# Kernel tuning notes

Hardware: AMD Instinct MI355X
Metric: run time of the kernel (lower is better)

The kernel has to match this reference:

```python
import jax, jax.numpy as jnp
import numpy as np

NG, NL, NCAM, NP, ED = 8, 4, 6, 7, 256  # groups, levels, cams, key points, embed dims
GD = ED // NG
FIX_SCALE = jnp.array([[0.0, 0.0, 0.0], [0.45, 0.0, 0.0], [-0.45, 0.0, 0.0],
                       [0.0, 0.45, 0.0], [0.0, -0.45, 0.0], [0.0, 0.0, 0.45],
                       [0.0, 0.0, -0.45]], dtype=jnp.float32)


def grid_sample_bilinear(feat, grid):
    """feat [N,C,H,W], grid [N,A,P,2] in [-1,1]; bilinear, zeros padding, align_corners=False."""
    N, C, H, W = feat.shape
    A, P = grid.shape[1], grid.shape[2]
    gx = (grid[..., 0] + 1.0) * (W * 0.5) - 0.5
    gy = (grid[..., 1] + 1.0) * (H * 0.5) - 0.5
    x0 = jnp.floor(gx)
    y0 = jnp.floor(gy)
    wx1 = gx - x0
    wy1 = gy - y0
    feat_flat = feat.reshape(N, C, H * W)

    def gather(xi, yi, w):
        valid = (xi >= 0) & (xi <= W - 1) & (yi >= 0) & (yi <= H - 1)
        xc = jnp.clip(xi, 0, W - 1).astype(jnp.int32)
        yc = jnp.clip(yi, 0, H - 1).astype(jnp.int32)
        idx = (yc * W + xc).reshape(N, 1, A * P)
        vals = jnp.take_along_axis(feat_flat, idx, axis=2)  # [N,C,A*P]
        return vals * (w * valid).reshape(N, 1, A * P)

    out = (gather(x0, y0, (1.0 - wx1) * (1.0 - wy1))
           + gather(x0 + 1.0, y0, wx1 * (1.0 - wy1))
           + gather(x0, y0 + 1.0, (1.0 - wx1) * wy1)
           + gather(x0 + 1.0, y0 + 1.0, wx1 * wy1))
    return out.reshape(N, C, A, P)


def _forward(instance_feature, anchor, anchor_embed, feat0, feat1, feat2, feat3,
             projection_mat, image_wh, w_fc, b_fc, w_out, b_out):
    B, A = anchor.shape[:2]
    # --- key point generation (box_code_size=8: size + yaw rotation + translation) ---
    size = jnp.exp(anchor[..., 3:6])[:, :, None, :]           # [B,A,1,3]
    kp = FIX_SCALE * size                                      # [B,A,7,3]
    sin, cos = anchor[..., 6], anchor[..., 7]
    z = jnp.zeros_like(cos)
    o = jnp.ones_like(cos)
    rot = jnp.stack([jnp.stack([cos, -sin, z], -1),
                     jnp.stack([sin, cos, z], -1),
                     jnp.stack([z, z, o], -1)], -2)            # [B,A,3,3]
    kp = jnp.einsum('baij,bapj->bapi', rot, kp) + anchor[..., None, 0:3]

    # --- attention weights: softmax over cams*levels*pts per group ---
    feature = instance_feature + anchor_embed
    w = feature @ w_fc.T + b_fc                                # [B,A,NG*NCAM*NL*NP]
    w = jax.nn.softmax(w.reshape(B, A, NCAM * NL * NP, NG), axis=2)
    w = w.reshape(B, A, NCAM, NL, NP, NG)

    # --- project key points to normalized image coords ---
    pts = jnp.concatenate([kp, jnp.ones_like(kp[..., :1])], -1)  # [B,A,7,4]
    p2d = jnp.einsum('bcij,bapj->bcapi', projection_mat, pts)[..., :3]
    xy = p2d[..., :2] / jnp.maximum(p2d[..., 2:3], 1e-5)
    xy = xy / jnp.maximum(image_wh[:, :, None, None], 1e-5)
    grid = (xy * 2.0 - 1.0).reshape(B * NCAM, A, NP, 2)

    # --- multilevel bilinear sampling ---
    levels = [feat0, feat1, feat2, feat3]
    sampled = jnp.stack([grid_sample_bilinear(f.reshape((B * NCAM,) + f.shape[2:]), grid)
                         for f in levels], axis=1)             # [B*Ncam,NL,C,A,P]
    feats = sampled.reshape(B, NCAM, NL, ED, A, NP).transpose(0, 4, 1, 2, 5, 3)  # [B,A,Ncam,NL,P,C]
    feats = feats.reshape(B, A, NCAM, NL, NP, NG, GD)

    # --- weighted fusion over cams, levels, then sum over key points ---
    fused = jnp.einsum('bacnpgd,bacnpg->bagd', feats, w).reshape(B, A, ED)
    return fused @ w_out.T + b_out


def setup_inputs() -> dict:
    ks = jax.random.split(jax.random.key(0), 13)
    B, A = 2, 900
    return {
        'instance_feature': jax.random.normal(ks[0], (B, A, ED), jnp.float32),
        'anchor': jax.random.normal(ks[1], (B, A, 8), jnp.float32),
        'anchor_embed': jax.random.normal(ks[2], (B, A, ED), jnp.float32),
        'feat0': jax.random.normal(ks[3], (B, NCAM, ED, 64, 176), jnp.float32),
        'feat1': jax.random.normal(ks[4], (B, NCAM, ED, 32, 88), jnp.float32),
        'feat2': jax.random.normal(ks[5], (B, NCAM, ED, 16, 44), jnp.float32),
        'feat3': jax.random.normal(ks[6], (B, NCAM, ED, 8, 22), jnp.float32),
        'projection_mat': jax.random.normal(ks[7], (B, NCAM, 4, 4), jnp.float32),
        'image_wh': jnp.ones((B, NCAM, 2), jnp.float32),
        'w_fc': jax.random.normal(ks[8], (NG * NCAM * NL * NP, ED), jnp.float32) * 0.02,
        'b_fc': jax.random.normal(ks[9], (NG * NCAM * NL * NP,), jnp.float32) * 0.02,
        'w_out': jax.random.normal(ks[10], (ED, ED), jnp.float32) * 0.02,
        'b_out': jax.random.normal(ks[11], (ED,), jnp.float32) * 0.02,
    }


def reference(instance_feature, anchor, anchor_embed, feat0, feat1, feat2, feat3,
              projection_mat, image_wh, w_fc, b_fc, w_out, b_out):
    return _forward(instance_feature, anchor, anchor_embed, feat0, feat1, feat2, feat3,
                    projection_mat, image_wh, w_fc, b_fc, w_out, b_out)
```

## Files before the change

### kernel.cpp

```cpp
#include <hip/hip_runtime.h>
#include <math.h>

constexpr int B = 2, A = 900, ED = 256, NG = 8, NCAM = 6, NL = 4, NP = 7;
constexpr int NJ = NG * NCAM * NL * NP;
constexpr int NBA = B * A;
constexpr int NE = NCAM * NL * NP;
constexpr int SPLIT = 2;
constexpr int EHALF = NE / SPLIT;

constexpr int NFCB = 225 * 7;
constexpr int TPB  = 935;
constexpr int NTRB = TPB * B * NCAM;

typedef float nfloat4 __attribute__((ext_vector_type(4)));

__constant__ float FIXS[NP][3] = {
  {0.f,0.f,0.f},{0.45f,0.f,0.f},{-0.45f,0.f,0.f},
  {0.f,0.45f,0.f},{0.f,-0.45f,0.f},{0.f,0.f,0.45f},{0.f,0.f,-0.45f}};

__constant__ int cH[NL]  = {64,32,16,8};
__constant__ int cW[NL]  = {176,88,44,22};
__constant__ int cHW[NL] = {11264,2816,704,176};
__constant__ long long cLOFF[NL] = {0LL, 34603008LL, 43253760LL, 45416448LL};

__global__ __launch_bounds__(256) void k_prep(
    const float* __restrict__ f0, const float* __restrict__ f1,
    const float* __restrict__ f2, const float* __restrict__ f3,
    const float* __restrict__ inst, const float* __restrict__ emb,
    const float* __restrict__ w_fc, const float* __restrict__ b_fc,
    float* __restrict__ tfeat, float* __restrict__ wraw)
{
  __shared__ float smem[4160];
  const int bid = blockIdx.x;
  const int t   = threadIdx.x;

  if (bid < NFCB) {
    float* fsh = smem;
    float* wts = smem + 2048;
    const int a0 = (bid / 7) * 8;
    const int j0 = (bid % 7) * 192;

    for (int i = t; i < 8 * ED; i += 256) {
      const int a = i >> 8, k = i & 255;
      const size_t idx = (size_t)(a0 + a) * ED + k;
      fsh[i] = inst[idx] + emb[idx];
    }

    float acc[8] = {0.f,0.f,0.f,0.f,0.f,0.f,0.f,0.f};
    for (int kc = 0; kc < 32; ++kc) {
      __syncthreads();
      for (int idx = t; idx < 384; idx += 256) {
        const int row = idx >> 1, q = idx & 1;
        const float4 v = *(const float4*)&w_fc[(size_t)(j0 + row)*ED + kc*8 + 4*q];
        wts[(4*q+0)*193 + row] = v.x;
        wts[(4*q+1)*193 + row] = v.y;
        wts[(4*q+2)*193 + row] = v.z;
        wts[(4*q+3)*193 + row] = v.w;
      }
      __syncthreads();
      if (t < 192) {
        const int kb = kc * 8;
#pragma unroll
        for (int k = 0; k < 8; k += 4) {
          const float w0 = wts[(k+0)*193 + t];
          const float w1 = wts[(k+1)*193 + t];
          const float w2 = wts[(k+2)*193 + t];
          const float w3 = wts[(k+3)*193 + t];
#pragma unroll
          for (int a = 0; a < 8; ++a)
            acc[a] += w0*fsh[a*ED + kb+k]   + w1*fsh[a*ED + kb+k+1]
                    + w2*fsh[a*ED + kb+k+2] + w3*fsh[a*ED + kb+k+3];
        }
      }
    }
    if (t < 192) {
      const int j = j0 + t;
      const float bj = b_fc[j];
#pragma unroll
      for (int a = 0; a < 8; ++a)
        wraw[(size_t)(a0+a)*NJ + j] = acc[a] + bj;
    }
    return;
  }

  const int fb = bid - NFCB;
  const int bc = fb / TPB;
  const int bx = fb % TPB;
  int lvl, px0, ch0;
  const float* src;
  if (bx < 704)      { lvl = 0; src = f0; px0 = (bx >> 2) * 64;         ch0 = (bx & 3) * 64; }
  else if (bx < 880) { lvl = 1; src = f1; px0 = ((bx - 704) >> 2) * 64; ch0 = ((bx - 704) & 3) * 64; }
  else if (bx < 924) { lvl = 2; src = f2; px0 = ((bx - 880) >> 2) * 64; ch0 = ((bx - 880) & 3) * 64; }
  else               { lvl = 3; src = f3; px0 = (bx - 924) * 16;        ch0 = 0; }
  const int HW = cHW[lvl];
  const float* in = src + (size_t)bc * ED * HW;
  float* outp = tfeat + cLOFF[lvl] + (size_t)bc * HW * ED;

  if (lvl < 3) {
    const int pxl = t & 15, cr = t >> 4;
#pragma unroll
    for (int i = 0; i < 4; ++i) {
      const int ch = cr + 16*i;
      const nfloat4 v = __builtin_nontemporal_load(
          reinterpret_cast<const nfloat4*>(in + (size_t)(ch0 + ch)*HW + px0 + 4*pxl));
      smem[(4*pxl+0)*65 + ch] = v.x;
      smem[(4*pxl+1)*65 + ch] = v.y;
      smem[(4*pxl+2)*65 + ch] = v.z;
      smem[(4*pxl+3)*65 + ch] = v.w;
    }
    __syncthreads();
    const int chl = t & 15, pw = t >> 4;
#pragma unroll
    for (int i = 0; i < 4; ++i) {
      const int px = pw + 16*i;
      nfloat4 v;
      v.x = smem[px*65 + 4*chl + 0];
      v.y = smem[px*65 + 4*chl + 1];
      v.z = smem[px*65 + 4*chl + 2];
      v.w = smem[px*65 + 4*chl + 3];
      __builtin_nontemporal_store(v,
          reinterpret_cast<nfloat4*>(outp + (size_t)(px0 + px)*ED + ch0 + 4*chl));
    }
  } else {
    const int pxl = t & 3, cr = t >> 2;
#pragma unroll
    for (int i = 0; i < 4; ++i) {
      const int ch = cr + 64*i;
      const nfloat4 v = __builtin_nontemporal_load(
          reinterpret_cast<const nfloat4*>(in + (size_t)ch*HW + px0 + 4*pxl));
      smem[(4*pxl+0)*257 + ch] = v.x;
      smem[(4*pxl+1)*257 + ch] = v.y;
      smem[(4*pxl+2)*257 + ch] = v.z;
      smem[(4*pxl+3)*257 + ch] = v.w;
    }
    __syncthreads();
    const int chl = t & 63, pw = t >> 6;
#pragma unroll
    for (int i = 0; i < 4; ++i) {
      const int px = pw + 4*i;
      nfloat4 v;
      v.x = smem[px*257 + 4*chl + 0];
      v.y = smem[px*257 + 4*chl + 1];
      v.z = smem[px*257 + 4*chl + 2];
      v.w = smem[px*257 + 4*chl + 3];
      __builtin_nontemporal_store(v,
          reinterpret_cast<nfloat4*>(outp + (size_t)(px0 + px)*ED + 4*chl));
    }
  }
}

template<bool CL>
__global__ __launch_bounds__(256) void k_sample_h(
    const float* __restrict__ anchor, const float* __restrict__ proj,
    const float* __restrict__ wh, const float* __restrict__ wraw,
    const float* __restrict__ tfeat,
    const float* __restrict__ f0, const float* __restrict__ f1,
    const float* __restrict__ f2, const float* __restrict__ f3,
    float* __restrict__ fused)
{
  __shared__ float wsh[NJ];
  __shared__ float gridsh[NCAM][NP][2];
  __shared__ const float* cptr[EHALF][4];
  __shared__ float4 cwt[EHALF];
  __shared__ int2   cmeta[EHALF];
  __shared__ int wcnt[4];

  const int ba   = blockIdx.x;
  const int half = blockIdx.y;
  const int b    = ba / A;
  const int t    = threadIdx.x;

  for (int j = t; j < NJ; j += 256)
    wsh[(j & 7) * NE + (j >> 3)] = wraw[(size_t)ba*NJ + j];

  if (t < NCAM*NP) {
    const int c = t / NP, p = t % NP;
    const float* an = anchor + (size_t)ba * 8;
    const float sx = expf(an[3]), sy = expf(an[4]), sz = expf(an[5]);
    const float sn = an[6], cs = an[7];
    const float kx = FIXS[p][0]*sx, ky = FIXS[p][1]*sy, kz = FIXS[p][2]*sz;
    const float px = cs*kx - sn*ky + an[0];
    const float py = sn*kx + cs*ky + an[1];
    const float pz = kz + an[2];
    const float* P = proj + ((size_t)(b*NCAM + c))*16;
    const float X = P[0]*px + P[1]*py + P[2]*pz  + P[3];
    const float Y = P[4]*px + P[5]*py + P[6]*pz  + P[7];
    const float Z = P[8]*px + P[9]*py + P[10]*pz + P[11];
    const float zc  = fmaxf(Z, 1e-5f);
    const float whx = fmaxf(wh[(b*NCAM+c)*2+0], 1e-5f);
    const float why = fmaxf(wh[(b*NCAM+c)*2+1], 1e-5f);
    gridsh[c][p][0] = (X/zc/whx)*2.f - 1.f;
    gridsh[c][p][1] = (Y/zc/why)*2.f - 1.f;
  }
  __syncthreads();

  bool valid = false;
  int chstep = 0;
  float4 w4 = make_float4(0.f,0.f,0.f,0.f);
  const float *p00=nullptr, *p10=nullptr, *p01=nullptr, *p11=nullptr;
  const int e = half * EHALF + t;
  if (t < EHALF) {
    const int c = e / (NL*NP); const int r = e % (NL*NP);
    const int l = r / NP, p = r % NP;
    const int Wl = cW[l], Hl = cH[l], HWl = cHW[l];
    const float gx = (gridsh[c][p][0] + 1.f) * (Wl * 0.5f) - 0.5f;
    const float gy = (gridsh[c][p][1] + 1.f) * (Hl * 0.5f) - 0.5f;
    const float x0f = floorf(gx), y0f = floorf(gy);
    const bool vx0 = (x0f >=  0.f) & (x0f <= (float)(Wl-1));
    const bool vx1 = (x0f >= -1.f) & (x0f <= (float)(Wl-2));
    const bool vy0 = (y0f >=  0.f) & (y0f <= (float)(Hl-1));
    const bool vy1 = (y0f >= -1.f) & (y0f <= (float)(Hl-2));
    if (vx0|vx1|vy0|vy1) {
      const float wx1 = gx - x0f, wy1 = gy - y0f;
      const int x0 = (int)fmaxf(fminf(x0f,        (float)(Wl-1)), 0.f);
      const int x1 = (int)fmaxf(fminf(x0f + 1.f,  (float)(Wl-1)), 0.f);
      const int y0 = (int)fmaxf(fminf(y0f,        (float)(Hl-1)), 0.f);
      const int y1 = (int)fmaxf(fminf(y0f + 1.f,  (float)(Hl-1)), 0.f);
      w4 = make_float4((1.f-wx1)*(1.f-wy1)*(vx0&&vy0),
                       wx1*(1.f-wy1)*(vx1&&vy0),
                       (1.f-wx1)*wy1*(vx0&&vy1),
                       wx1*wy1*(vx1&&vy1));
      if (w4.x != 0.f || w4.y != 0.f || w4.z != 0.f || w4.w != 0.f) {
        const float* base;
        int estep;
        if (CL) {
          base = tfeat + cLOFF[l] + (size_t)(b*NCAM + c) * HWl * ED;
          estep = ED; chstep = 1;
        } else {
          const float* fp = (l==0)?f0:(l==1)?f1:(l==2)?f2:f3;
          base = fp + (size_t)(b*NCAM + c) * ED * HWl;
          estep = 1; chstep = HWl;
        }
        p00 = base + (size_t)(y0*Wl + x0) * estep;
        p10 = base + (size_t)(y0*Wl + x1) * estep;
        p01 = base + (size_t)(y1*Wl + x0) * estep;
        p11 = base + (size_t)(y1*Wl + x1) * estep;
        valid = true;
      }
    }
  }

  const unsigned long long mask = __ballot(valid);
  const int lane = t & 63, wv = t >> 6;
  if (lane == 0) wcnt[wv] = __popcll(mask);
  __syncthreads();
  int off = 0, nv = 0;
#pragma unroll
  for (int i = 0; i < 4; ++i) { if (i < wv) off += wcnt[i]; nv += wcnt[i]; }
  if (valid) {
    const int pos = off + __popcll(mask & ((1ull << lane) - 1ull));
    cptr[pos][0] = p00; cptr[pos][1] = p10; cptr[pos][2] = p01; cptr[pos][3] = p11;
    cwt[pos]   = w4;
    cmeta[pos] = make_int2(chstep, e);
  }

  {
    const int g = t >> 5, ln = t & 31;
    float* wg = wsh + g * NE;
    float m = -3.4e38f;
    for (int i = ln; i < NE; i += 32) m = fmaxf(m, wg[i]);
#pragma unroll
    for (int mk = 16; mk >= 1; mk >>= 1) m = fmaxf(m, __shfl_xor(m, mk));
    float s = 0.f;
    for (int i = ln; i < NE; i += 32) {
      const float ev = expf(wg[i] - m);
      wg[i] = ev;
      s += ev;
    }
#pragma unroll
    for (int mk = 16; mk >= 1; mk >>= 1) s += __shfl_xor(s, mk);
    const float inv = 1.f / s;
    for (int i = ln; i < NE; i += 32) wg[i] *= inv;
  }
  __syncthreads();

  float acc = 0.f;
  const int g = t >> 5;
#pragma unroll 4
  for (int i = 0; i < nv; ++i) {
    const int2 m = cmeta[i];
    const size_t toff = (size_t)t * m.x;
    const float4 w = cwt[i];
    const float aw = wsh[g*NE + m.y];
    const float v00 = cptr[i][0][toff];
    const float v10 = cptr[i][1][toff];
    const float v01 = cptr[i][2][toff];
    const float v11 = cptr[i][3][toff];
    acc += aw * (w.x*v00 + w.y*v10 + w.z*v01 + w.w*v11);
  }
  fused[((size_t)half * NBA + ba) * ED + t] = acc;
}

__global__ __launch_bounds__(256) void k_out(const float* __restrict__ fused,
    const float* __restrict__ w_out, const float* __restrict__ b_out,
    float* __restrict__ out)
{
  __shared__ float fsh[8][ED];
  const int a0 = blockIdx.x * 8;
  const int t = threadIdx.x;
#pragma unroll
  for (int k = 0; k < 8; ++k)
    fsh[k][t] = fused[(size_t)(a0+k)*ED + t]
              + fused[(size_t)NBA*ED + (size_t)(a0+k)*ED + t];
  __syncthreads();
  float acc[8] = {0.f,0.f,0.f,0.f,0.f,0.f,0.f,0.f};
  for (int i = 0; i < ED; i += 4) {
    const float4 w4 = *(const float4*)&w_out[(size_t)t*ED + i];
#pragma unroll
    for (int k = 0; k < 8; ++k) {
      const float4 fv = *(const float4*)&fsh[k][i];
      acc[k] += w4.x*fv.x + w4.y*fv.y + w4.z*fv.z + w4.w*fv.w;
    }
  }
  const float bo = b_out[t];
#pragma unroll
  for (int k = 0; k < 8; ++k) out[(size_t)(a0+k)*ED + t] = acc[k] + bo;
}

extern "C" void kernel_launch(void* const* d_in, const int* in_sizes, int n_in,
                              void* d_out, int out_size, void* d_ws, size_t ws_size,
                              hipStream_t stream) {
  const float* inst   = (const float*)d_in[0];
  const float* anchor = (const float*)d_in[1];
  const float* emb    = (const float*)d_in[2];
  const float* f0 = (const float*)d_in[3];
  const float* f1 = (const float*)d_in[4];
  const float* f2 = (const float*)d_in[5];
  const float* f3 = (const float*)d_in[6];
  const float* proj  = (const float*)d_in[7];
  const float* wh    = (const float*)d_in[8];
  const float* w_fc  = (const float*)d_in[9];
  const float* b_fc  = (const float*)d_in[10];
  const float* w_out = (const float*)d_in[11];
  const float* b_out = (const float*)d_in[12];
  float* out = (float*)d_out;
  float* ws  = (float*)d_ws;

  const size_t TFEAT = 45957120ULL;
  const size_t WRAW  = (size_t)NBA * NJ;
  const size_t FUSED = (size_t)SPLIT * NBA * ED;
  const bool tr = ws_size >= (TFEAT + WRAW + FUSED) * sizeof(float);

  float* tfeat  = ws;
  float* wraw   = tr ? (ws + TFEAT) : ws;
  float* fusedp = wraw + WRAW;

  k_prep<<<NFCB + (tr ? NTRB : 0), 256, 0, stream>>>(f0, f1, f2, f3,
      inst, emb, w_fc, b_fc, tfeat, wraw);

  if (tr)
    k_sample_h<true><<<dim3(NBA, SPLIT), 256, 0, stream>>>(anchor, proj, wh,
        wraw, tfeat, f0, f1, f2, f3, fusedp);
  else
    k_sample_h<false><<<dim3(NBA, SPLIT), 256, 0, stream>>>(anchor, proj, wh,
        wraw, tfeat, f0, f1, f2, f3, fusedp);

  k_out<<<NBA / 8, 256, 0, stream>>>(fusedp, w_out, b_out, out);
}
```

Baseline: 342.8 us.

## Process two transpose tiles per block with overlapped loads and widen FC k-chunks

The feature transpose now handles two tiles per block, issuing the second tile's global loads while the first tile's stores go out, and launches half as many transpose blocks. Shared memory is doubled to hold both tiles. The FC projection part now stages 32 k-values per chunk instead of 8, which cuts the number of barriers per block. Nontemporal loads are also replaced by plain loads. The larger LDS footprint may reduce occupancy for both block types.

Result: slower. 396.0 us (+15.5%).

```diff
diff --git a/kernel.cpp b/kernel.cpp
--- a/kernel.cpp
+++ b/kernel.cpp
@@ -8,9 +8,10 @@
 constexpr int SPLIT = 2;
 constexpr int EHALF = NE / SPLIT;
 
-constexpr int NFCB = 225 * 7;
-constexpr int TPB  = 935;
-constexpr int NTRB = TPB * B * NCAM;
+constexpr int NFCB  = 225 * 7;
+constexpr int TPB   = 935;
+constexpr int NTRB  = TPB * B * NCAM;
+constexpr int NTRB2 = NTRB / 2;
 
 typedef float nfloat4 __attribute__((ext_vector_type(4)));
 
@@ -22,6 +23,99 @@
 __constant__ int cW[NL]  = {176,88,44,22};
 __constant__ int cHW[NL] = {11264,2816,704,176};
 __constant__ long long cLOFF[NL] = {0LL, 34603008LL, 43253760LL, 45416448LL};
+
+struct TI { const float* inb; float* outb; int px0, ch0, HW; bool big; };
+
+__device__ __forceinline__ TI tile_info(int tt,
+    const float* f0, const float* f1, const float* f2, const float* f3,
+    float* tfeat)
+{
+  TI ti;
+  const int bc = tt / TPB;
+  const int bx = tt % TPB;
+  int lvl;
+  const float* src;
+  if (bx < 704)      { lvl = 0; src = f0; ti.px0 = (bx >> 2) * 64;         ti.ch0 = (bx & 3) * 64; }
+  else if (bx < 880) { lvl = 1; src = f1; ti.px0 = ((bx - 704) >> 2) * 64; ti.ch0 = ((bx - 704) & 3) * 64; }
+  else if (bx < 924) { lvl = 2; src = f2; ti.px0 = ((bx - 880) >> 2) * 64; ti.ch0 = ((bx - 880) & 3) * 64; }
+  else               { lvl = 3; src = f3; ti.px0 = (bx - 924) * 16;        ti.ch0 = 0; }
+  ti.HW  = cHW[lvl];
+  ti.big = (lvl < 3);
+  ti.inb  = src + (size_t)bc * ED * ti.HW;
+  ti.outb = tfeat + cLOFF[lvl] + (size_t)bc * ti.HW * ED;
+  return ti;
+}
+
+__device__ __forceinline__ void tile_load(const TI& ti, int t, nfloat4 r[4]) {
+  if (ti.big) {
+    const int pxl = t & 15, cr = t >> 4;
+#pragma unroll
+    for (int i = 0; i < 4; ++i)
+      r[i] = *reinterpret_cast<const nfloat4*>(
+          ti.inb + (size_t)(ti.ch0 + cr + 16*i)*ti.HW + ti.px0 + 4*pxl);
+  } else {
+    const int pxl = t & 3, cr = t >> 2;
+#pragma unroll
+    for (int i = 0; i < 4; ++i)
+      r[i] = *reinterpret_cast<const nfloat4*>(
+          ti.inb + (size_t)(cr + 64*i)*ti.HW + ti.px0 + 4*pxl);
+  }
+}
+
+__device__ __forceinline__ void tile_lds(float* buf, const TI& ti, int t,
+                                         const nfloat4 r[4]) {
+  if (ti.big) {
+    const int pxl = t & 15, cr = t >> 4;
+#pragma unroll
+    for (int i = 0; i < 4; ++i) {
+      const int ch = cr + 16*i;
+      buf[(4*pxl+0)*65 + ch] = r[i].x;
+      buf[(4*pxl+1)*65 + ch] = r[i].y;
+      buf[(4*pxl+2)*65 + ch] = r[i].z;
+      buf[(4*pxl+3)*65 + ch] = r[i].w;
+    }
+  } else {
+    const int pxl = t & 3, cr = t >> 2;
+#pragma unroll
+    for (int i = 0; i < 4; ++i) {
+      const int ch = cr + 64*i;
+      buf[(4*pxl+0)*257 + ch] = r[i].x;
+      buf[(4*pxl+1)*257 + ch] = r[i].y;
+      buf[(4*pxl+2)*257 + ch] = r[i].z;
+      buf[(4*pxl+3)*257 + ch] = r[i].w;
+    }
+  }
+}
+
+__device__ __forceinline__ void tile_store(const float* buf, const TI& ti, int t) {
+  if (ti.big) {
+    const int chl = t & 15, pw = t >> 4;
+#pragma unroll
+    for (int i = 0; i < 4; ++i) {
+      const int px = pw + 16*i;
+      nfloat4 v;
+      v.x = buf[px*65 + 4*chl + 0];
+      v.y = buf[px*65 + 4*chl + 1];
+      v.z = buf[px*65 + 4*chl + 2];
+      v.w = buf[px*65 + 4*chl + 3];
+      __builtin_nontemporal_store(v, reinterpret_cast<nfloat4*>(
+          ti.outb + (size_t)(ti.px0 + px)*ED + ti.ch0 + 4*chl));
+    }
+  } else {
+    const int chl = t & 63, pw = t >> 6;
+#pragma unroll
+    for (int i = 0; i < 4; ++i) {
+      const int px = pw + 4*i;
+      nfloat4 v;
+      v.x = buf[px*257 + 4*chl + 0];
+      v.y = buf[px*257 + 4*chl + 1];
+      v.z = buf[px*257 + 4*chl + 2];
+      v.w = buf[px*257 + 4*chl + 3];
+      __builtin_nontemporal_store(v, reinterpret_cast<nfloat4*>(
+          ti.outb + (size_t)(ti.px0 + px)*ED + 4*chl));
+    }
+  }
+}
 
 __global__ __launch_bounds__(256) void k_prep(
     const float* __restrict__ f0, const float* __restrict__ f1,
@@ -30,7 +124,7 @@
     const float* __restrict__ w_fc, const float* __restrict__ b_fc,
     float* __restrict__ tfeat, float* __restrict__ wraw)
 {
-  __shared__ float smem[4160];
+  __shared__ float smem[8320];
   const int bid = blockIdx.x;
   const int t   = threadIdx.x;
 
@@ -47,11 +141,11 @@
     }
 
     float acc[8] = {0.f,0.f,0.f,0.f,0.f,0.f,0.f,0.f};
-    for (int kc = 0; kc < 32; ++kc) {
+    for (int kc = 0; kc < 8; ++kc) {
       __syncthreads();
-      for (int idx = t; idx < 384; idx += 256) {
-        const int row = idx >> 1, q = idx & 1;
-        const float4 v = *(const float4*)&w_fc[(size_t)(j0 + row)*ED + kc*8 + 4*q];
+      for (int idx = t; idx < 1536; idx += 256) {
+        const int row = idx >> 3, q = idx & 7;
+        const float4 v = *(const float4*)&w_fc[(size_t)(j0 + row)*ED + kc*32 + 4*q];
         wts[(4*q+0)*193 + row] = v.x;
         wts[(4*q+1)*193 + row] = v.y;
         wts[(4*q+2)*193 + row] = v.z;
@@ -59,17 +153,17 @@
       }
       __syncthreads();
       if (t < 192) {
-        const int kb = kc * 8;
-#pragma unroll
-        for (int k = 0; k < 8; k += 4) {
+#pragma unroll
+        for (int k = 0; k < 32; k += 4) {
           const float w0 = wts[(k+0)*193 + t];
           const float w1 = wts[(k+1)*193 + t];
           const float w2 = wts[(k+2)*193 + t];
           const float w3 = wts[(k+3)*193 + t];
+          const int kb = kc * 32 + k;
 #pragma unroll
           for (int a = 0; a < 8; ++a)
-            acc[a] += w0*fsh[a*ED + kb+k]   + w1*fsh[a*ED + kb+k+1]
-                    + w2*fsh[a*ED + kb+k+2] + w3*fsh[a*ED + kb+k+3];
+            acc[a] += w0*fsh[a*ED + kb]   + w1*fsh[a*ED + kb+1]
+                    + w2*fsh[a*ED + kb+2] + w3*fsh[a*ED + kb+3];
         }
       }
     }
@@ -84,69 +178,20 @@
   }
 
   const int fb = bid - NFCB;
-  const int bc = fb / TPB;
-  const int bx = fb % TPB;
-  int lvl, px0, ch0;
-  const float* src;
-  if (bx < 704)      { lvl = 0; src = f0; px0 = (bx >> 2) * 64;         ch0 = (bx & 3) * 64; }
-  else if (bx < 880) { lvl = 1; src = f1; px0 = ((bx - 704) >> 2) * 64; ch0 = ((bx - 704) & 3) * 64; }
-  else if (bx < 924) { lvl = 2; src = f2; px0 = ((bx - 880) >> 2) * 64; ch0 = ((bx - 880) & 3) * 64; }
-  else               { lvl = 3; src = f3; px0 = (bx - 924) * 16;        ch0 = 0; }
-  const int HW = cHW[lvl];
-  const float* in = src + (size_t)bc * ED * HW;
-  float* outp = tfeat + cLOFF[lvl] + (size_t)bc * HW * ED;
-
-  if (lvl < 3) {
-    const int pxl = t & 15, cr = t >> 4;
-#pragma unroll
-    for (int i = 0; i < 4; ++i) {
-      const int ch = cr + 16*i;
-      const nfloat4 v = __builtin_nontemporal_load(
-          reinterpret_cast<const nfloat4*>(in + (size_t)(ch0 + ch)*HW + px0 + 4*pxl));
-      smem[(4*pxl+0)*65 + ch] = v.x;
-      smem[(4*pxl+1)*65 + ch] = v.y;
-      smem[(4*pxl+2)*65 + ch] = v.z;
-      smem[(4*pxl+3)*65 + ch] = v.w;
-    }
-    __syncthreads();
-    const int chl = t & 15, pw = t >> 4;
-#pragma unroll
-    for (int i = 0; i < 4; ++i) {
-      const int px = pw + 16*i;
-      nfloat4 v;
-      v.x = smem[px*65 + 4*chl + 0];
-      v.y = smem[px*65 + 4*chl + 1];
-      v.z = smem[px*65 + 4*chl + 2];
-      v.w = smem[px*65 + 4*chl + 3];
-      __builtin_nontemporal_store(v,
-          reinterpret_cast<nfloat4*>(outp + (size_t)(px0 + px)*ED + ch0 + 4*chl));
-    }
-  } else {
-    const int pxl = t & 3, cr = t >> 2;
-#pragma unroll
-    for (int i = 0; i < 4; ++i) {
-      const int ch = cr + 64*i;
-      const nfloat4 v = __builtin_nontemporal_load(
-          reinterpret_cast<const nfloat4*>(in + (size_t)ch*HW + px0 + 4*pxl));
-      smem[(4*pxl+0)*257 + ch] = v.x;
-      smem[(4*pxl+1)*257 + ch] = v.y;
-      smem[(4*pxl+2)*257 + ch] = v.z;
-      smem[(4*pxl+3)*257 + ch] = v.w;
-    }
-    __syncthreads();
-    const int chl = t & 63, pw = t >> 6;
-#pragma unroll
-    for (int i = 0; i < 4; ++i) {
-      const int px = pw + 4*i;
-      nfloat4 v;
-      v.x = smem[px*257 + 4*chl + 0];
-      v.y = smem[px*257 + 4*chl + 1];
-      v.z = smem[px*257 + 4*chl + 2];
-      v.w = smem[px*257 + 4*chl + 3];
-      __builtin_nontemporal_store(v,
-          reinterpret_cast<nfloat4*>(outp + (size_t)(px0 + px)*ED + 4*chl));
-    }
-  }
+  const TI Ati = tile_info(2*fb + 0, f0, f1, f2, f3, tfeat);
+  const TI Bti = tile_info(2*fb + 1, f0, f1, f2, f3, tfeat);
+  float* bufA = smem;
+  float* bufB = smem + 4160;
+
+  nfloat4 ra[4], rb[4];
+  tile_load(Ati, t, ra);
+  tile_lds(bufA, Ati, t, ra);
+  __syncthreads();
+  tile_load(Bti, t, rb);
+  tile_store(bufA, Ati, t);
+  tile_lds(bufB, Bti, t, rb);
+  __syncthreads();
+  tile_store(bufB, Bti, t);
 }
 
 template<bool CL>
@@ -345,7 +390,7 @@
   float* wraw   = tr ? (ws + TFEAT) : ws;
   float* fusedp = wraw + WRAW;
 
-  k_prep<<<NFCB + (tr ? NTRB : 0), 256, 0, stream>>>(f0, f1, f2, f3,
+  k_prep<<<NFCB + (tr ? NTRB2 : 0), 256, 0, stream>>>(f0, f1, f2, f3,
       inst, emb, w_fc, b_fc, tfeat, wraw);
 
   if (tr)
```
